# Kernel optimization log

Measured on AMD Instinct MI355X. Metric: run time of the kernel, lower is better.

Reference implementation:

```python
import jax, jax.numpy as jnp
import numpy as np

FEAT_STRIDE = 16
PRE_NMS_TOPN = 6000
POST_NMS_TOPN = 300
NMS_THRESH = 0.7
MIN_SIZE = 16.0
NEG = -1e9


def _whctrs(a):
    w = a[2] - a[0] + 1.0
    h = a[3] - a[1] + 1.0
    return w, h, a[0] + 0.5 * (w - 1), a[1] + 0.5 * (h - 1)


def _mkanchors(ws, hs, xc, yc):
    return np.stack([xc - 0.5 * (ws - 1), yc - 0.5 * (hs - 1),
                     xc + 0.5 * (ws - 1), yc + 0.5 * (hs - 1)], axis=1)


def generate_anchors(base_size=16, ratios=(0.5, 1.0, 2.0), scales=(8, 16, 32)):
    base = np.array([0, 0, base_size - 1, base_size - 1], dtype=np.float64)
    w, h, xc, yc = _whctrs(base)
    size = w * h
    ratios = np.array(ratios, dtype=np.float64)
    ws = np.round(np.sqrt(size / ratios))
    hs = np.round(ws * ratios)
    ratio_anchors = _mkanchors(ws, hs, xc, yc)
    out = []
    for a in ratio_anchors:
        w, h, xc, yc = _whctrs(a)
        s = np.array(scales, dtype=np.float64)
        out.append(_mkanchors(w * s, h * s, xc, yc))
    return np.concatenate(out, axis=0).astype(np.float32)


def _nms_single(boxes, scores):
    # boxes [N,4], scores [N] (sorted desc by top_k); greedy NMS, fixed POST_NMS_TOPN picks
    x1, y1, x2, y2 = boxes[:, 0], boxes[:, 1], boxes[:, 2], boxes[:, 3]
    areas = (x2 - x1 + 1.0) * (y2 - y1 + 1.0)

    def body(i, st):
        keep, ok, live = st
        s = jnp.where(live, scores, NEG - 1.0)
        j = jnp.argmax(s)
        valid = s[j] > NEG / 2
        keep = keep.at[i].set(j.astype(jnp.int32))
        ok = ok.at[i].set(valid)
        xx1 = jnp.maximum(x1[j], x1)
        yy1 = jnp.maximum(y1[j], y1)
        xx2 = jnp.minimum(x2[j], x2)
        yy2 = jnp.minimum(y2[j], y2)
        inter = jnp.maximum(xx2 - xx1 + 1.0, 0.0) * jnp.maximum(yy2 - yy1 + 1.0, 0.0)
        iou = inter / (areas[j] + areas - inter)
        live = live & (iou <= NMS_THRESH)
        return keep, ok, live

    keep0 = jnp.zeros((POST_NMS_TOPN,), jnp.int32)
    ok0 = jnp.zeros((POST_NMS_TOPN,), bool)
    live0 = scores > NEG / 2
    keep, ok, _ = jax.lax.fori_loop(0, POST_NMS_TOPN, body, (keep0, ok0, live0))
    return keep, ok


def _proposals(rpn_cls_prob, rpn_bbox_pred, im_info, anchors):
    B, _, H, W = rpn_cls_prob.shape
    A = anchors.shape[0]
    # fg scores: second half of the 2A channel dim
    scores = rpn_cls_prob[:, A:].transpose(0, 2, 3, 1).reshape(B, -1)          # [B, H*W*A]
    deltas = rpn_bbox_pred.transpose(0, 2, 3, 1).reshape(B, -1, 4)             # [B, H*W*A, 4]
    # shifted anchors over the feature map
    sx = (jnp.arange(W, dtype=jnp.float32)) * FEAT_STRIDE
    sy = (jnp.arange(H, dtype=jnp.float32)) * FEAT_STRIDE
    gx, gy = jnp.meshgrid(sx, sy)                                              # [H, W]
    shifts = jnp.stack([gx.ravel(), gy.ravel(), gx.ravel(), gy.ravel()], 1)    # [K, 4]
    all_anchors = (shifts[:, None, :] + anchors[None, :, :]).reshape(-1, 4)    # [K*A, 4]
    # bbox_transform_inv
    wa = all_anchors[:, 2] - all_anchors[:, 0] + 1.0
    ha = all_anchors[:, 3] - all_anchors[:, 1] + 1.0
    cxa = all_anchors[:, 0] + 0.5 * (wa - 1.0)
    cya = all_anchors[:, 1] + 0.5 * (ha - 1.0)
    dx, dy, dw, dh = deltas[..., 0], deltas[..., 1], deltas[..., 2], deltas[..., 3]
    cx = dx * wa + cxa
    cy = dy * ha + cya
    pw = jnp.exp(dw) * wa
    ph = jnp.exp(dh) * ha
    x1 = cx - 0.5 * (pw - 1.0)
    y1 = cy - 0.5 * (ph - 1.0)
    x2 = cx + 0.5 * (pw - 1.0)
    y2 = cy + 0.5 * (ph - 1.0)
    # clip to image
    imh = im_info[:, 0:1]
    imw = im_info[:, 1:2]
    x1 = jnp.clip(x1, 0.0, imw - 1.0)
    y1 = jnp.clip(y1, 0.0, imh - 1.0)
    x2 = jnp.clip(x2, 0.0, imw - 1.0)
    y2 = jnp.clip(y2, 0.0, imh - 1.0)
    boxes = jnp.stack([x1, y1, x2, y2], axis=-1)                               # [B, N, 4]
    # filter boxes smaller than min_size * im_scale (mask by score)
    min_sz = MIN_SIZE * im_info[:, 2:3]
    keep_m = ((x2 - x1 + 1.0) >= min_sz) & ((y2 - y1 + 1.0) >= min_sz)
    scores = jnp.where(keep_m, scores, NEG)
    # pre-NMS top-k
    scores_top, order = jax.lax.top_k(scores, PRE_NMS_TOPN)                    # [B, 6000]
    boxes_top = jnp.take_along_axis(boxes, order[:, :, None], axis=1)          # [B, 6000, 4]
    # greedy NMS per image
    keep, keep_ok = jax.vmap(_nms_single)(boxes_top, scores_top)               # [B, 300]
    sel = jnp.take_along_axis(boxes_top, keep[:, :, None], axis=1)             # [B, 300, 4]
    sel = jnp.where(keep_ok[:, :, None], sel, 0.0)
    bidx = jnp.broadcast_to(jnp.arange(B, dtype=sel.dtype)[:, None, None], (B, POST_NMS_TOPN, 1))
    return jnp.concatenate([bidx, sel], axis=-1)                               # [B, 300, 5]


def setup_inputs() -> dict:
    key = jax.random.key(0)
    k1, k2 = jax.random.split(key)
    B, H, W, A = 32, 100, 100, 9
    rpn_cls_prob = jax.random.uniform(k1, (B, 2 * A, H, W), dtype=jnp.float32)
    rpn_bbox_pred = jax.random.normal(k2, (B, 4 * A, H, W), dtype=jnp.float32) * 0.2
    im_info = jnp.tile(jnp.array([[1600.0, 1600.0, 1.0]], dtype=jnp.float32), (B, 1))
    anchors = jnp.asarray(generate_anchors(base_size=16, ratios=(0.5, 1.0, 2.0), scales=(8, 16, 32)))
    return {"rpn_cls_prob": rpn_cls_prob, "rpn_bbox_pred": rpn_bbox_pred,
            "im_info": im_info, "anchors": anchors}


def reference(rpn_cls_prob, rpn_bbox_pred, im_info, anchors):
    return _proposals(rpn_cls_prob, rpn_bbox_pred, im_info, anchors)
```

## Files before the change

### kernel.cpp

```cpp
#include <hip/hip_runtime.h>

#define NB 32
#define NA 9
#define FH 100
#define FW 100
#define HWSZ (FH*FW)
#define NANCH (HWSZ*NA)
#define PRE 6000
#define POST 300
#define SORTN 8192
#define NEGV -1000000000.0f
#define NMS_T 0.7f
#define MARG 1e-4f
#define NCHUNK ((PRE + 63) / 64)
#define SW(i) ((i) ^ (((i) >> 4) & 7))
#define WB() __builtin_amdgcn_wave_barrier()
#define NSLICE 11
#define DSLICE 8192

typedef unsigned long long u64;
typedef unsigned int u32;

__device__ __forceinline__ u32 f2sort(float f) {
  u32 u = __float_as_uint(f);
  return (u & 0x80000000u) ? ~u : (u | 0x80000000u);
}

__device__ __forceinline__ float4 decode_box(const float* __restrict__ pred,
                                             const float* __restrict__ anchors,
                                             int b, int i, float imw, float imh) {
  int hw = i / NA; int a = i - hw * NA;
  int h = hw / FW; int w = hw - h * FW;
  float sx = (float)(w * 16);
  float sy = (float)(h * 16);
  float ax1 = anchors[a*4+0] + sx, ay1 = anchors[a*4+1] + sy;
  float ax2 = anchors[a*4+2] + sx, ay2 = anchors[a*4+3] + sy;
  float wa = ax2 - ax1 + 1.0f, ha = ay2 - ay1 + 1.0f;
  float cxa = ax1 + 0.5f*(wa - 1.0f), cya = ay1 + 0.5f*(ha - 1.0f);
  size_t base = (((size_t)b*36 + a*4)*FH + h)*FW + w;
  float dx = pred[base];
  float dy = pred[base + HWSZ];
  float dw = pred[base + 2*HWSZ];
  float dh = pred[base + 3*HWSZ];
  float cx = dx*wa + cxa, cy = dy*ha + cya;
  float pw = expf(dw)*wa, ph = expf(dh)*ha;
  float x1 = fminf(fmaxf(cx - 0.5f*(pw - 1.0f), 0.0f), imw - 1.0f);
  float y1 = fminf(fmaxf(cy - 0.5f*(ph - 1.0f), 0.0f), imh - 1.0f);
  float x2 = fminf(fmaxf(cx + 0.5f*(pw - 1.0f), 0.0f), imw - 1.0f);
  float y2 = fminf(fmaxf(cy + 0.5f*(ph - 1.0f), 0.0f), imh - 1.0f);
  return make_float4(x1, y1, x2, y2);
}

__global__ void k_zero(u32* __restrict__ histg) {
  int i = blockIdx.x * 1024 + threadIdx.x;
  if (i < NB * 4096) histg[i] = 0;
}

__global__ __launch_bounds__(1024) void k_decode(
    const float* __restrict__ cls,
    const float* __restrict__ pred,
    const float* __restrict__ iminfo,
    const float* __restrict__ anchors,
    u32* __restrict__ scoreg,
    u32* __restrict__ histg) {
  __shared__ u32 hl[4096];
  const int blk = blockIdx.x;
  const int b = blk / NSLICE, s = blk - b * NSLICE;
  const int tid = threadIdx.x;
  for (int j = tid; j < 4096; j += 1024) hl[j] = 0;
  __syncthreads();
  const float imh = iminfo[b*3+0], imw = iminfo[b*3+1], sc = iminfo[b*3+2];
  const float msz = 16.0f * sc;
  #pragma unroll
  for (int r = 0; r < 8; ++r) {
    int i = s * DSLICE + r * 1024 + tid;
    if (i < NANCH) {
      int hw = i / NA; int a = i - hw * NA;
      int h = hw / FW; int w = hw - h * FW;
      float score = cls[(((size_t)b*18 + 9 + a)*FH + h)*FW + w];
      float4 bx = decode_box(pred, anchors, b, i, imw, imh);
      bool keep = ((bx.z - bx.x + 1.0f) >= msz) && ((bx.w - bx.y + 1.0f) >= msz);
      float sf = keep ? score : NEGV;
      float t = sf * 4096.0f;
      int bin = (t <= 0.0f) ? 0 : ((t >= 4095.0f) ? 4095 : (int)t);
      atomicAdd(&hl[bin], 1u);
      scoreg[(size_t)b * NANCH + i] = f2sort(sf);
    }
  }
  __syncthreads();
  for (int j = tid; j < 4096; j += 1024) {
    u32 v = hl[j];
    if (v) atomicAdd(&histg[b * 4096 + j], v);
  }
}

__device__ __forceinline__ void w0_cut(u32* hist, u32 target, int lane,
                                       int* cutBin) {
  u32 cs = 0;
  int cb = lane * 64;
  for (int i = 0; i < 64; ++i) cs += hist[cb + ((i + lane) & 63)];
  u32 suf = cs;
  #pragma unroll
  for (int d = 1; d < 64; d <<= 1) {
    u32 o = __shfl_down(suf, (unsigned)d, 64);
    suf += (lane < 64 - d) ? o : 0u;
  }
  u64 m1 = __ballot(suf >= target);
  int L = 63 - __clzll(m1);
  u32 nAb = (L < 63) ? (u32)__builtin_amdgcn_readlane((int)suf, L + 1) : 0u;
  u32 fs = hist[L * 64 + lane];
  #pragma unroll
  for (int d = 1; d < 64; d <<= 1) {
    u32 o = __shfl_down(fs, (unsigned)d, 64);
    fs += (lane < 64 - d) ? o : 0u;
  }
  fs += nAb;
  u64 m2 = __ballot(fs >= target);
  int fb = 63 - __clzll(m2);
  *cutBin = L * 64 + fb;
}

#define CEX(A,B,UP) { if ((UP) ? ((A) > (B)) : ((A) < (B))) { u64 _t=(A); (A)=(B); (B)=_t; } }

#define SMEM_BYTES 103424
__global__ __launch_bounds__(1024, 1) void k_fused(
    const u32* __restrict__ scoreg,
    const u32* __restrict__ histg,
    const float* __restrict__ pred,
    const float* __restrict__ iminfo,
    const float* __restrict__ anchors,
    float* __restrict__ out) {
  __shared__ __align__(16) unsigned char smemRaw[SMEM_BYTES];
  u64* cand = (u64*)smemRaw;
  u32* histL = (u32*)(smemRaw + 65536);
  float4* boxes = (float4*)smemRaw;
  u64* liveM = (u64*)(smemRaw + 96256);
  float4* accB = (float4*)(smemRaw + 97024);
  float* accA = (float*)(smemRaw + 101824);
  u64* okm = (u64*)(smemRaw + 103040);
  int* scal = (int*)(smemRaw + 103168);
  float* aL = (float*)(smemRaw + 103232);

  const int b = blockIdx.x;
  const int tid = threadIdx.x;
  const int wave = tid >> 6, lane = tid & 63;
  const u32* sb = scoreg + (size_t)b * NANCH;
  const u32 liveThr = f2sort(-5.0e8f);

  if (tid < 36) aL[tid] = anchors[tid];
  for (int j = tid; j < 4096; j += 1024) histL[j] = histg[b * 4096 + j];
  if (tid == 0) scal[0] = 0;
  __syncthreads();
  if (wave == 0) {
    int L;
    w0_cut(histL, PRE, lane, &L);
    if (lane == 0) scal[1] = L;
  }
  __syncthreads();
  const u32 thrT = f2sort((float)scal[1] * (1.0f / 4096.0f));

  const uint4* sb4 = (const uint4*)sb;
  for (int t = 0; t < 22; ++t) {
    int vi = t * 1024 + tid;
    bool inb = vi < 22500;
    uint4 v = inb ? sb4[vi] : make_uint4(0, 0, 0, 0);
    int i0 = vi * 4;
    #pragma unroll
    for (int c = 0; c < 4; ++c) {
      u32 s = (&v.x)[c];
      bool p = inb && (s >= thrT);
      u64 bal = __ballot(p);
      int cnt = __popcll(bal);
      int base = 0;
      if (lane == 0 && cnt) base = atomicAdd(&scal[0], cnt);
      base = __builtin_amdgcn_readfirstlane(base);
      int pos = base + __popcll(bal & ((1ull << lane) - 1ull));
      if (p && pos < SORTN) cand[SW(pos)] = ((u64)s << 32) | (u32)(~(u32)(i0 + c));
    }
  }
  __syncthreads();
  {
    int cnt = scal[0]; if (cnt > SORTN) cnt = SORTN;
    for (int i = tid; i < SORTN; i += 1024)
      if (i >= cnt) cand[SW(i)] = 0ull;
  }
  __syncthreads();

  {
    int tb = tid * 8;
    u64 e0=cand[SW(tb+0)], e1=cand[SW(tb+1)], e2=cand[SW(tb+2)], e3=cand[SW(tb+3)];
    u64 e4=cand[SW(tb+4)], e5=cand[SW(tb+5)], e6=cand[SW(tb+6)], e7=cand[SW(tb+7)];
    bool u8b = (tb & 8) != 0;
    CEX(e0,e1,false) CEX(e2,e3,true) CEX(e4,e5,false) CEX(e6,e7,true)
    CEX(e0,e2,false) CEX(e1,e3,false) CEX(e4,e6,true) CEX(e5,e7,true)
    CEX(e0,e1,false) CEX(e2,e3,false) CEX(e4,e5,true) CEX(e6,e7,true)
    CEX(e0,e4,u8b) CEX(e1,e5,u8b) CEX(e2,e6,u8b) CEX(e3,e7,u8b)
    CEX(e0,e2,u8b) CEX(e1,e3,u8b) CEX(e4,e6,u8b) CEX(e5,e7,u8b)
    CEX(e0,e1,u8b) CEX(e2,e3,u8b) CEX(e4,e5,u8b) CEX(e6,e7,u8b)
    cand[SW(tb+0)]=e0; cand[SW(tb+1)]=e1; cand[SW(tb+2)]=e2; cand[SW(tb+3)]=e3;
    cand[SW(tb+4)]=e4; cand[SW(tb+5)]=e5; cand[SW(tb+6)]=e6; cand[SW(tb+7)]=e7;
    WB();
  }
  for (int k = 16; k <= SORTN; k <<= 1) {
    int j = k >> 1;
    for (; j >= 512; j >>= 1) {
      __syncthreads();
      for (int m = tid; m < SORTN/2; m += 1024) {
        int i = ((m & ~(j-1)) << 1) | (m & (j-1));
        int x = i | j;
        u64 a0 = cand[SW(i)], a1 = cand[SW(x)];
        bool up = (i & k) != 0;
        if (up ? (a0 > a1) : (a0 < a1)) { cand[SW(i)] = a1; cand[SW(x)] = a0; }
      }
    }
    if (k >= 1024) __syncthreads();
    for (; j >= 8; j >>= 1) {
      int base = wave * 512;
      for (int m = lane; m < 256; m += 64) {
        int lo = ((m & ~(j-1)) << 1) | (m & (j-1));
        int i = base + lo, x = i | j;
        u64 a0 = cand[SW(i)], a1 = cand[SW(x)];
        bool up = (i & k) != 0;
        if (up ? (a0 > a1) : (a0 < a1)) { cand[SW(i)] = a1; cand[SW(x)] = a0; }
      }
      WB();
    }
    {
      int tb = tid * 8;
      u64 e0=cand[SW(tb+0)], e1=cand[SW(tb+1)], e2=cand[SW(tb+2)], e3=cand[SW(tb+3)];
      u64 e4=cand[SW(tb+4)], e5=cand[SW(tb+5)], e6=cand[SW(tb+6)], e7=cand[SW(tb+7)];
      bool up = (tb & k) != 0;
      CEX(e0,e4,up) CEX(e1,e5,up) CEX(e2,e6,up) CEX(e3,e7,up)
      CEX(e0,e2,up) CEX(e1,e3,up) CEX(e4,e6,up) CEX(e5,e7,up)
      CEX(e0,e1,up) CEX(e2,e3,up) CEX(e4,e5,up) CEX(e6,e7,up)
      cand[SW(tb+0)]=e0; cand[SW(tb+1)]=e1; cand[SW(tb+2)]=e2; cand[SW(tb+3)]=e3;
      cand[SW(tb+4)]=e4; cand[SW(tb+5)]=e5; cand[SW(tb+6)]=e6; cand[SW(tb+7)]=e7;
      WB();
    }
  }
  __syncthreads();

  const float imh = iminfo[b*3+0], imw = iminfo[b*3+1];
  u64 ce[6];
  #pragma unroll
  for (int r = 0; r < 6; ++r) {
    int i = tid + 1024 * r;
    ce[r] = (i < NCHUNK*64) ? cand[SW(i)] : 0ull;
  }
  __syncthreads();
  #pragma unroll
  for (int r = 0; r < 6; ++r) {
    int c = wave + 16 * r;
    if (c < NCHUNK) {
      int i = tid + 1024 * r;
      u64 k = ce[r];
      int idx = (int)(~(u32)k);
      bool v = (u32)idx < (u32)NANCH;
      bool live = ((u32)(k >> 32) > liveThr) && v && (i < PRE);
      int id = v ? idx : 0;
      int hw = id / NA; int a = id - hw * NA;
      int h = hw / FW; int w = hw - h * FW;
      float sx = (float)(w * 16), sy = (float)(h * 16);
      float ax1 = aL[a*4+0] + sx, ay1 = aL[a*4+1] + sy;
      float ax2 = aL[a*4+2] + sx, ay2 = aL[a*4+3] + sy;
      float wa = ax2 - ax1 + 1.0f, ha = ay2 - ay1 + 1.0f;
      float cxa = ax1 + 0.5f*(wa - 1.0f), cya = ay1 + 0.5f*(ha - 1.0f);
      size_t base = (((size_t)b*36 + a*4)*FH + h)*FW + w;
      float dx = pred[base], dy = pred[base + HWSZ];
      float dw = pred[base + 2*HWSZ], dh = pred[base + 3*HWSZ];
      float cx = dx*wa + cxa, cy = dy*ha + cya;
      float pw = expf(dw)*wa, ph = expf(dh)*ha;
      float4 bc;
      bc.x = fminf(fmaxf(cx - 0.5f*(pw - 1.0f), 0.0f), imw - 1.0f);
      bc.y = fminf(fmaxf(cy - 0.5f*(ph - 1.0f), 0.0f), imh - 1.0f);
      bc.z = fminf(fmaxf(cx + 0.5f*(pw - 1.0f), 0.0f), imw - 1.0f);
      bc.w = fminf(fmaxf(cy + 0.5f*(ph - 1.0f), 0.0f), imh - 1.0f);
      boxes[i] = bc;
      u64 lm = __ballot(live);
      if (lane == 0) liveM[c] = lm;
    }
  }
  if (tid == 0) scal[4] = 0;
  __syncthreads();

  for (int g = 0; g < NCHUNK; ++g) {
    int nA = scal[4];
    if (nA >= POST) break;
    u64 lm = liveM[g];
    if (lm == 0ull) continue;
    float4 bc = boxes[g * 64 + lane];
    float areaC = (bc.z - bc.x + 1.0f) * (bc.w - bc.y + 1.0f);
    bool ok = (lm >> lane) & 1ull;
    for (int tt = wave; tt < nA; tt += 16) {
      if (__ballot(ok) == 0ull) break;
      float4 ba = accB[tt];
      float aA = accA[tt];
      float xx1 = fmaxf(ba.x, bc.x);
      float yy1 = fmaxf(ba.y, bc.y);
      float xx2 = fminf(ba.z, bc.z);
      float yy2 = fminf(ba.w, bc.w);
      float inter = fmaxf(xx2 - xx1 + 1.0f, 0.0f) * fmaxf(yy2 - yy1 + 1.0f, 0.0f);
      float un = aA + areaC - inter;
      float q = inter * __builtin_amdgcn_rcpf(un);
      bool hi = q > NMS_T + MARG;
      bool lo = q < NMS_T - MARG;
      bool sup = hi;
      if (__ballot(ok && !hi && !lo)) {
        if (!hi && !lo) sup = (inter / un) > NMS_T;
      }
      ok = ok && !sup;
    }
    u64 wm = __ballot(ok);
    if (lane == 0) okm[wave] = wm;
    __syncthreads();
    if (wave == 0) {
      u64 m = okm[0];
      #pragma unroll
      for (int w = 1; w < 16; ++w) m &= okm[w];
      bool ok0 = (m >> lane) & 1ull;
      int nAcc = nA;
      u64 bal = __ballot(ok0);
      while (bal != 0ull && nAcc < POST) {
        int fl = __ffsll(bal) - 1;
        float ax1 = __int_as_float(__builtin_amdgcn_readlane(__float_as_int(bc.x), fl));
        float ay1 = __int_as_float(__builtin_amdgcn_readlane(__float_as_int(bc.y), fl));
        float ax2 = __int_as_float(__builtin_amdgcn_readlane(__float_as_int(bc.z), fl));
        float ay2 = __int_as_float(__builtin_amdgcn_readlane(__float_as_int(bc.w), fl));
        float aA = (ax2 - ax1 + 1.0f) * (ay2 - ay1 + 1.0f);
        if (lane == 0) { accB[nAcc] = make_float4(ax1, ay1, ax2, ay2); accA[nAcc] = aA; }
        ++nAcc;
        if (ok0) {
          if (lane == fl) ok0 = false;
          else if (lane > fl) {
            float xx1 = fmaxf(ax1, bc.x);
            float yy1 = fmaxf(ay1, bc.y);
            float xx2 = fminf(ax2, bc.z);
            float yy2 = fminf(ay2, bc.w);
            float inter = fmaxf(xx2 - xx1 + 1.0f, 0.0f) * fmaxf(yy2 - yy1 + 1.0f, 0.0f);
            float iou = inter / (aA + areaC - inter);
            if (iou > NMS_T) ok0 = false;
          }
        }
        bal = __ballot(ok0);
      }
      if (lane == 0) scal[4] = nAcc;
    }
    __syncthreads();
  }

  const int nAcc = scal[4];
  float* ob = out + (size_t)b * POST * 5;
  for (int i = tid; i < POST * 5; i += 1024) {
    int row = i / 5, col = i - row * 5;
    float v = 0.f;
    if (col == 0) v = (float)b;
    else if (row < nAcc) {
      float4 bb = accB[row];
      v = (col == 1) ? bb.x : (col == 2) ? bb.y : (col == 3) ? bb.z : bb.w;
    }
    ob[i] = v;
  }
}

extern "C" void kernel_launch(void* const* d_in, const int* in_sizes, int n_in,
                              void* d_out, int out_size, void* d_ws, size_t ws_size,
                              hipStream_t stream) {
  const float* cls     = (const float*)d_in[0];
  const float* pred    = (const float*)d_in[1];
  const float* iminfo  = (const float*)d_in[2];
  const float* anchors = (const float*)d_in[3];
  float* out = (float*)d_out;

  u32* histg  = (u32*)d_ws;
  u32* scoreg = (u32*)((char*)d_ws + 524288);

  k_zero<<<(NB*4096 + 1023)/1024, 1024, 0, stream>>>(histg);
  k_decode<<<NB*NSLICE, 1024, 0, stream>>>(cls, pred, iminfo, anchors, scoreg, histg);
  k_fused<<<NB, 1024, 0, stream>>>(scoreg, histg, pred, iminfo, anchors, out);
}
```

Measured before the change: 238.8 us.

## Replace per-batch bitonic sort with histogram bucket scatter and per-bin sorts

Result: faster. 206.3 us (-13.6%).

```diff
diff --git a/kernel.cpp b/kernel.cpp
--- a/kernel.cpp
+++ b/kernel.cpp
@@ -13,7 +13,6 @@
 #define NMS_T 0.7f
 #define MARG 1e-4f
 #define NCHUNK ((PRE + 63) / 64)
-#define SW(i) ((i) ^ (((i) >> 4) & 7))
 #define WB() __builtin_amdgcn_wave_barrier()
 #define NSLICE 11
 #define DSLICE 8192
@@ -51,9 +50,10 @@
   return make_float4(x1, y1, x2, y2);
 }
 
-__global__ void k_zero(u32* __restrict__ histg) {
+__global__ void k_zero(u32* __restrict__ histcnt, u32* __restrict__ cand32) {
   int i = blockIdx.x * 1024 + threadIdx.x;
-  if (i < NB * 4096) histg[i] = 0;
+  if (i < 262144) histcnt[i] = 0;
+  cand32[i] = 0;
 }
 
 __global__ __launch_bounds__(1024) void k_decode(
@@ -120,19 +120,116 @@
   *cutBin = L * 64 + fb;
 }
 
-#define CEX(A,B,UP) { if ((UP) ? ((A) > (B)) : ((A) < (B))) { u64 _t=(A); (A)=(B); (B)=_t; } }
+__global__ __launch_bounds__(64) void k_cut(const u32* __restrict__ histg,
+                                            u32* __restrict__ thrTg,
+                                            u32* __restrict__ binStartG) {
+  __shared__ u32 hl[4096];
+  const int b = blockIdx.x, lane = threadIdx.x;
+  const u32* h = histg + b * 4096;
+  for (int i = lane; i < 4096; i += 64) hl[i] = h[i];
+  __syncthreads();
+  int L;
+  w0_cut(hl, PRE, lane, &L);
+  u32 running = 0;
+  for (int hi = 4095; hi >= L; hi -= 64) {
+    int bin = hi - lane;
+    u32 c = (bin >= L && bin >= 0) ? hl[bin] : 0u;
+    u32 p = c;
+    #pragma unroll
+    for (int d = 1; d < 64; d <<= 1) {
+      u32 o = __shfl_up(p, (unsigned)d, 64);
+      if (lane >= d) p += o;
+    }
+    if (bin >= L && bin >= 0) binStartG[b * 4096 + bin] = running + p - c;
+    running += (u32)__builtin_amdgcn_readlane((int)p, 63);
+  }
+  if (lane == 0) thrTg[b] = f2sort((float)L * (1.0f / 4096.0f));
+}
+
+__global__ __launch_bounds__(1024) void k_scatter(
+    const u32* __restrict__ scoreg,
+    const u32* __restrict__ thrTg,
+    const u32* __restrict__ binStartG,
+    u32* __restrict__ binCntG,
+    u64* __restrict__ candg) {
+  const int blk = blockIdx.x;
+  const int b = blk / NSLICE, s = blk - b * NSLICE;
+  const int tid = threadIdx.x;
+  const u32 thrT = thrTg[b];
+  const u32* sb = scoreg + (size_t)b * NANCH;
+  #pragma unroll
+  for (int r = 0; r < 8; ++r) {
+    int i = s * DSLICE + r * 1024 + tid;
+    if (i < NANCH) {
+      u32 sv = sb[i];
+      if (sv >= thrT) {
+        float f = __uint_as_float(sv ^ 0x80000000u);
+        float t = f * 4096.0f;
+        int bin = (t >= 4095.0f) ? 4095 : (int)t;
+        u32 pos = binStartG[b * 4096 + bin] + atomicAdd(&binCntG[b * 4096 + bin], 1u);
+        if (pos < SORTN) candg[(size_t)b * SORTN + pos] = ((u64)sv << 32) | (u32)(~(u32)i);
+      }
+    }
+  }
+}
+
+__global__ __launch_bounds__(1024) void k_binsort(
+    const u32* __restrict__ binStartG,
+    const u32* __restrict__ binCntG,
+    u64* __restrict__ candg) {
+  __shared__ u64 sc[16][512];
+  const int wave = threadIdx.x >> 6, lane = threadIdx.x & 63;
+  const int task = blockIdx.x * 16 + wave;
+  const int b = task >> 12, bin = task & 4095;
+  u32 cnt = binCntG[b * 4096 + bin];
+  if (cnt < 2) return;
+  u32 base = binStartG[b * 4096 + bin];
+  if (base >= SORTN) return;
+  u32 m = cnt;
+  if (base + m > SORTN) m = SORTN - base;
+  u64* seg = candg + (size_t)b * SORTN + base;
+  if (m <= 64) {
+    u64 v = (lane < (int)m) ? seg[lane] : 0ull;
+    #pragma unroll
+    for (int k = 2; k <= 64; k <<= 1) {
+      for (int j = k >> 1; j > 0; j >>= 1) {
+        u64 o = __shfl_xor((unsigned long long)v, j, 64);
+        bool dirD = ((lane & k) == 0);
+        bool lower = ((lane & j) == 0);
+        bool takeMax = (dirD == lower);
+        bool sw = takeMax ? (o > v) : (o < v);
+        if (sw) v = o;
+      }
+    }
+    if (lane < (int)m) seg[lane] = v;
+  } else if (m <= 512) {
+    int np = 128; while (np < (int)m) np <<= 1;
+    for (int i = lane; i < np; i += 64) sc[wave][i] = (i < (int)m) ? seg[i] : 0ull;
+    WB();
+    for (int k = 2; k <= np; k <<= 1) {
+      for (int j = k >> 1; j > 0; j >>= 1) {
+        for (int q = lane; q < np/2; q += 64) {
+          int i = ((q & ~(j-1)) << 1) | (q & (j-1));
+          int x = i | j;
+          u64 a0 = sc[wave][i], a1 = sc[wave][x];
+          bool up = (i & k) != 0;
+          if (up ? (a0 > a1) : (a0 < a1)) { sc[wave][i] = a1; sc[wave][x] = a0; }
+        }
+        WB();
+      }
+    }
+    for (int i = lane; i < (int)m; i += 64) seg[i] = sc[wave][i];
+  }
+}
 
 #define SMEM_BYTES 103424
-__global__ __launch_bounds__(1024, 1) void k_fused(
-    const u32* __restrict__ scoreg,
-    const u32* __restrict__ histg,
+__global__ __launch_bounds__(1024, 1) void k_nms(
+    const u64* __restrict__ candg,
     const float* __restrict__ pred,
     const float* __restrict__ iminfo,
     const float* __restrict__ anchors,
     float* __restrict__ out) {
   __shared__ __align__(16) unsigned char smemRaw[SMEM_BYTES];
-  u64* cand = (u64*)smemRaw;
-  u32* histL = (u32*)(smemRaw + 65536);
   float4* boxes = (float4*)smemRaw;
   u64* liveM = (u64*)(smemRaw + 96256);
   float4* accB = (float4*)(smemRaw + 97024);
@@ -144,116 +241,20 @@
   const int b = blockIdx.x;
   const int tid = threadIdx.x;
   const int wave = tid >> 6, lane = tid & 63;
-  const u32* sb = scoreg + (size_t)b * NANCH;
   const u32 liveThr = f2sort(-5.0e8f);
+  const u64* cb = candg + (size_t)b * SORTN;
 
   if (tid < 36) aL[tid] = anchors[tid];
-  for (int j = tid; j < 4096; j += 1024) histL[j] = histg[b * 4096 + j];
-  if (tid == 0) scal[0] = 0;
-  __syncthreads();
-  if (wave == 0) {
-    int L;
-    w0_cut(histL, PRE, lane, &L);
-    if (lane == 0) scal[1] = L;
-  }
-  __syncthreads();
-  const u32 thrT = f2sort((float)scal[1] * (1.0f / 4096.0f));
-
-  const uint4* sb4 = (const uint4*)sb;
-  for (int t = 0; t < 22; ++t) {
-    int vi = t * 1024 + tid;
-    bool inb = vi < 22500;
-    uint4 v = inb ? sb4[vi] : make_uint4(0, 0, 0, 0);
-    int i0 = vi * 4;
-    #pragma unroll
-    for (int c = 0; c < 4; ++c) {
-      u32 s = (&v.x)[c];
-      bool p = inb && (s >= thrT);
-      u64 bal = __ballot(p);
-      int cnt = __popcll(bal);
-      int base = 0;
-      if (lane == 0 && cnt) base = atomicAdd(&scal[0], cnt);
-      base = __builtin_amdgcn_readfirstlane(base);
-      int pos = base + __popcll(bal & ((1ull << lane) - 1ull));
-      if (p && pos < SORTN) cand[SW(pos)] = ((u64)s << 32) | (u32)(~(u32)(i0 + c));
-    }
-  }
-  __syncthreads();
-  {
-    int cnt = scal[0]; if (cnt > SORTN) cnt = SORTN;
-    for (int i = tid; i < SORTN; i += 1024)
-      if (i >= cnt) cand[SW(i)] = 0ull;
-  }
-  __syncthreads();
-
-  {
-    int tb = tid * 8;
-    u64 e0=cand[SW(tb+0)], e1=cand[SW(tb+1)], e2=cand[SW(tb+2)], e3=cand[SW(tb+3)];
-    u64 e4=cand[SW(tb+4)], e5=cand[SW(tb+5)], e6=cand[SW(tb+6)], e7=cand[SW(tb+7)];
-    bool u8b = (tb & 8) != 0;
-    CEX(e0,e1,false) CEX(e2,e3,true) CEX(e4,e5,false) CEX(e6,e7,true)
-    CEX(e0,e2,false) CEX(e1,e3,false) CEX(e4,e6,true) CEX(e5,e7,true)
-    CEX(e0,e1,false) CEX(e2,e3,false) CEX(e4,e5,true) CEX(e6,e7,true)
-    CEX(e0,e4,u8b) CEX(e1,e5,u8b) CEX(e2,e6,u8b) CEX(e3,e7,u8b)
-    CEX(e0,e2,u8b) CEX(e1,e3,u8b) CEX(e4,e6,u8b) CEX(e5,e7,u8b)
-    CEX(e0,e1,u8b) CEX(e2,e3,u8b) CEX(e4,e5,u8b) CEX(e6,e7,u8b)
-    cand[SW(tb+0)]=e0; cand[SW(tb+1)]=e1; cand[SW(tb+2)]=e2; cand[SW(tb+3)]=e3;
-    cand[SW(tb+4)]=e4; cand[SW(tb+5)]=e5; cand[SW(tb+6)]=e6; cand[SW(tb+7)]=e7;
-    WB();
-  }
-  for (int k = 16; k <= SORTN; k <<= 1) {
-    int j = k >> 1;
-    for (; j >= 512; j >>= 1) {
-      __syncthreads();
-      for (int m = tid; m < SORTN/2; m += 1024) {
-        int i = ((m & ~(j-1)) << 1) | (m & (j-1));
-        int x = i | j;
-        u64 a0 = cand[SW(i)], a1 = cand[SW(x)];
-        bool up = (i & k) != 0;
-        if (up ? (a0 > a1) : (a0 < a1)) { cand[SW(i)] = a1; cand[SW(x)] = a0; }
-      }
-    }
-    if (k >= 1024) __syncthreads();
-    for (; j >= 8; j >>= 1) {
-      int base = wave * 512;
-      for (int m = lane; m < 256; m += 64) {
-        int lo = ((m & ~(j-1)) << 1) | (m & (j-1));
-        int i = base + lo, x = i | j;
-        u64 a0 = cand[SW(i)], a1 = cand[SW(x)];
-        bool up = (i & k) != 0;
-        if (up ? (a0 > a1) : (a0 < a1)) { cand[SW(i)] = a1; cand[SW(x)] = a0; }
-      }
-      WB();
-    }
-    {
-      int tb = tid * 8;
-      u64 e0=cand[SW(tb+0)], e1=cand[SW(tb+1)], e2=cand[SW(tb+2)], e3=cand[SW(tb+3)];
-      u64 e4=cand[SW(tb+4)], e5=cand[SW(tb+5)], e6=cand[SW(tb+6)], e7=cand[SW(tb+7)];
-      bool up = (tb & k) != 0;
-      CEX(e0,e4,up) CEX(e1,e5,up) CEX(e2,e6,up) CEX(e3,e7,up)
-      CEX(e0,e2,up) CEX(e1,e3,up) CEX(e4,e6,up) CEX(e5,e7,up)
-      CEX(e0,e1,up) CEX(e2,e3,up) CEX(e4,e5,up) CEX(e6,e7,up)
-      cand[SW(tb+0)]=e0; cand[SW(tb+1)]=e1; cand[SW(tb+2)]=e2; cand[SW(tb+3)]=e3;
-      cand[SW(tb+4)]=e4; cand[SW(tb+5)]=e5; cand[SW(tb+6)]=e6; cand[SW(tb+7)]=e7;
-      WB();
-    }
-  }
+  if (tid == 0) scal[4] = 0;
   __syncthreads();
 
   const float imh = iminfo[b*3+0], imw = iminfo[b*3+1];
-  u64 ce[6];
-  #pragma unroll
-  for (int r = 0; r < 6; ++r) {
-    int i = tid + 1024 * r;
-    ce[r] = (i < NCHUNK*64) ? cand[SW(i)] : 0ull;
-  }
-  __syncthreads();
   #pragma unroll
   for (int r = 0; r < 6; ++r) {
     int c = wave + 16 * r;
     if (c < NCHUNK) {
       int i = tid + 1024 * r;
-      u64 k = ce[r];
+      u64 k = cb[i];
       int idx = (int)(~(u32)k);
       bool v = (u32)idx < (u32)NANCH;
       bool live = ((u32)(k >> 32) > liveThr) && v && (i < PRE);
@@ -280,7 +281,6 @@
       if (lane == 0) liveM[c] = lm;
     }
   }
-  if (tid == 0) scal[4] = 0;
   __syncthreads();
 
   for (int g = 0; g < NCHUNK; ++g) {
@@ -292,7 +292,6 @@
     float areaC = (bc.z - bc.x + 1.0f) * (bc.w - bc.y + 1.0f);
     bool ok = (lm >> lane) & 1ull;
     for (int tt = wave; tt < nA; tt += 16) {
-      if (__ballot(ok) == 0ull) break;
       float4 ba = accB[tt];
       float aA = accA[tt];
       float xx1 = fmaxf(ba.x, bc.x);
@@ -371,10 +370,18 @@
   const float* anchors = (const float*)d_in[3];
   float* out = (float*)d_out;
 
-  u32* histg  = (u32*)d_ws;
-  u32* scoreg = (u32*)((char*)d_ws + 524288);
-
-  k_zero<<<(NB*4096 + 1023)/1024, 1024, 0, stream>>>(histg);
+  char* ws = (char*)d_ws;
+  u32* histg     = (u32*)(ws + 0);
+  u32* binCntG   = (u32*)(ws + 524288);
+  u32* binStartG = (u32*)(ws + 1048576);
+  u32* thrTg     = (u32*)(ws + 1572864);
+  u64* candg     = (u64*)(ws + 1572992);
+  u32* scoreg    = (u32*)(ws + 3670144);
+
+  k_zero<<<1024, 1024, 0, stream>>>(histg, (u32*)candg);
   k_decode<<<NB*NSLICE, 1024, 0, stream>>>(cls, pred, iminfo, anchors, scoreg, histg);
-  k_fused<<<NB, 1024, 0, stream>>>(scoreg, histg, pred, iminfo, anchors, out);
-}
+  k_cut<<<NB, 64, 0, stream>>>(histg, thrTg, binStartG);
+  k_scatter<<<NB*NSLICE, 1024, 0, stream>>>(scoreg, thrTg, binStartG, binCntG, candg);
+  k_binsort<<<8192, 1024, 0, stream>>>(binStartG, binCntG, candg);
+  k_nms<<<NB, 1024, 0, stream>>>(candg, pred, iminfo, anchors, out);
+}
```
